# Kernel tuning notes

Measured on AMD Instinct MI355X. Metric: run time of the kernel, lower is better.

## Reference

```python
import jax, jax.numpy as jnp
import numpy as np
from jax import lax

B, H, W = 1024, 28, 28
STEPS, KMAX = 32, 2
OUT_F, NUM_CLASSES = 32, 10
P = H * W  # 784 flattened filtration values
TSEQ1 = jnp.linspace(0.01, 0.29, STEPS, dtype=jnp.float32)
TSEQ2 = jnp.linspace(0.05, 0.3, STEPS, dtype=jnp.float32)
DN = ('NHWC', 'HWIO', 'NHWC')


def setup_inputs() -> dict:
    key = jax.random.key(0)
    ks = jax.random.split(key, 16)
    return {
        'x': jax.random.normal(ks[0], (B, H, W, 1), jnp.float32),
        'x_dtm005': jax.random.uniform(ks[1], (B, H, W, 1), jnp.float32, 0.0, 0.3),
        'x_dtm02': jax.random.uniform(ks[2], (B, H, W, 1), jnp.float32, 0.0, 0.3),
        'conv_w1': jax.random.normal(ks[3], (3, 3, 1, 32), jnp.float32) * 0.1,
        'conv_b1': jnp.zeros((32,), jnp.float32),
        'conv_w2': jax.random.normal(ks[4], (3, 3, 32, 1), jnp.float32) * 0.1,
        'conv_b2': jnp.zeros((1,), jnp.float32),
        'g1_w': jax.random.normal(ks[5], (KMAX * STEPS, OUT_F), jnp.float32) * 0.1,
        'g1_b': jnp.zeros((OUT_F,), jnp.float32),
        'g2_w': jax.random.normal(ks[6], (KMAX * STEPS, OUT_F), jnp.float32) * 0.1,
        'g2_b': jnp.zeros((OUT_F,), jnp.float32),
        'fc1_w': jax.random.normal(ks[7], (P + 2 * OUT_F, 64), jnp.float32) * 0.05,
        'fc1_b': jnp.zeros((64,), jnp.float32),
        'fc2_w': jax.random.normal(ks[8], (64, NUM_CLASSES), jnp.float32) * 0.1,
        'fc2_b': jnp.zeros((NUM_CLASSES,), jnp.float32),
    }


def _landscape(v, tseq):
    """Persistence landscape over a grid of t-values.

    v: [B, P] filtration (DTM) values; each value is a birth time, paired
    with a per-sample death at the max filtration value (sublevel sweep).
    Landscape lambda_k(t) = k-th largest tent max(0, min(t-b, d-t)).
    Returns [B, KMAX*STEPS].
    """
    death = jnp.max(v, axis=1)                                     # [B]
    # tent: [B, T, P]
    tent = jnp.maximum(0.0, jnp.minimum(tseq[None, :, None] - v[:, None, :],
                                        death[:, None, None] - tseq[None, :, None]))
    top = lax.top_k(tent, KMAX)[0]                                 # [B, T, K]
    return jnp.transpose(top, (0, 2, 1)).reshape(v.shape[0], KMAX * tseq.shape[0])


def reference(x, x_dtm005, x_dtm02, conv_w1, conv_b1, conv_w2, conv_b2,
              g1_w, g1_b, g2_w, g2_b, fc1_w, fc1_b, fc2_w, fc2_b):
    b = x.shape[0]
    # TDA branch 1 (sublevel=True -> no negation)
    x1 = _landscape(x_dtm005.reshape(b, -1), TSEQ1)
    x1 = jax.nn.relu(x1 @ g1_w + g1_b)
    # TDA branch 2
    x2 = _landscape(x_dtm02.reshape(b, -1), TSEQ2)
    x2 = jax.nn.relu(x2 @ g2_w + g2_b)
    # CNN branch: Conv(32) -> ReLU -> Conv(1), then extra ReLU per call()
    h = lax.conv_general_dilated(x, conv_w1, (1, 1), 'SAME', dimension_numbers=DN) + conv_b1
    h = jax.nn.relu(h)
    h = lax.conv_general_dilated(h, conv_w2, (1, 1), 'SAME', dimension_numbers=DN) + conv_b2
    h = jax.nn.relu(h)
    hf = h.reshape(b, -1)                                          # [B, 784]
    z = jnp.concatenate([hf, x1, x2], axis=-1)                     # [B, 848]
    z = jax.nn.relu(z @ fc1_w + fc1_b)
    return z @ fc2_w + fc2_b                                       # [B, 10]
```

## Files before the change

### kernel.cpp

```cpp
#include <hip/hip_runtime.h>

#define BATCH 1024
#define PP 784

__device__ __forceinline__ float dpp_wave_shr1(float v) {
  return __int_as_float(__builtin_amdgcn_update_dpp(
      0, __float_as_int(v), 0x138, 0xF, 0xF, true));
}
__device__ __forceinline__ float dpp_wave_shl1(float v) {
  return __int_as_float(__builtin_amdgcn_update_dpp(
      0, __float_as_int(v), 0x130, 0xF, 0xF, true));
}

__global__ __launch_bounds__(512, 6) void fused_kernel(
    const float* __restrict__ xin,
    const float* __restrict__ dtm1, const float* __restrict__ dtm2,
    const float* __restrict__ w1g, const float* __restrict__ b1g,
    const float* __restrict__ w2g, const float* __restrict__ b2g,
    const float* __restrict__ g1w, const float* __restrict__ g1b,
    const float* __restrict__ g2w, const float* __restrict__ g2b,
    const float* __restrict__ fc1w, const float* __restrict__ fc1b,
    const float* __restrict__ fc2w, const float* __restrict__ fc2b,
    float* __restrict__ out)
{
  const int b = blockIdx.x;
  const int tid = threadIdx.x;
  const int w = tid >> 6;
  const int lane = tid & 63;
  const int x = lane & 31;

  __shared__ float inL[28][36];
  __shared__ __align__(16) float wTL[2][32][12];
  __shared__ float b1L[32];
  __shared__ __align__(16) float pL[8][28][28];
  __shared__ __align__(16) float zL[864];
  __shared__ float red[2][8][3];

  for (int i = tid; i < 224; i += 512) {
    int y = i >> 3, k = i & 7;
    inL[y][k == 0 ? 0 : 28 + k] = 0.f;
  }
  for (int i = tid; i < 784; i += 512)
    inL[i / 28][i % 28 + 1] = xin[b * PP + i];
  for (int i = tid; i < 288; i += 512) {
    int c = i & 31, t = i >> 5;
    wTL[0][c][t] = w1g[i];
    wTL[1][c][t] = w2g[i];
  }
  if (tid < 32) b1L[tid] = b1g[tid];
  __syncthreads();

  {
    const int sub = lane >> 5;
    float4 waA[2], waB[2], wbA[2], wbB[2];
    float wa8[2], wb8[2], bb[2];
#pragma unroll
    for (int cp = 0; cp < 2; ++cp) {
      const int c = (w << 2) + (cp << 1) + sub;
      const float* p1 = &wTL[0][c][0];
      const float* p2 = &wTL[1][c][0];
      waA[cp] = *(const float4*)p1; waB[cp] = *(const float4*)(p1 + 4); wa8[cp] = p1[8];
      wbA[cp] = *(const float4*)p2; wbB[cp] = *(const float4*)(p2 + 4); wb8[cp] = p2[8];
      bb[cp] = b1L[c];
    }

    float A0 = 0.f, A1 = 0.f, A2 = 0.f;
    float B0 = inL[0][x], B1 = inL[0][x + 1], B2 = inL[0][x + 2];
    float aM = 0.f, aC = 0.f, aP = 0.f;

#pragma unroll 2
    for (int y = 0; y < 28; ++y) {
      float C0, C1, C2;
      if (y < 27) {
        C0 = inL[y + 1][x]; C1 = inL[y + 1][x + 1]; C2 = inL[y + 1][x + 2];
      } else { C0 = 0.f; C1 = 0.f; C2 = 0.f; }

#pragma unroll
      for (int cp = 0; cp < 2; ++cp) {
        float h = bb[cp];
        h = fmaf(A0, waA[cp].x, h); h = fmaf(A1, waA[cp].y, h); h = fmaf(A2, waA[cp].z, h);
        h = fmaf(B0, waA[cp].w, h); h = fmaf(B1, waB[cp].x, h); h = fmaf(B2, waB[cp].y, h);
        h = fmaf(C0, waB[cp].z, h); h = fmaf(C1, waB[cp].w, h); h = fmaf(C2, wa8[cp], h);
        h = (x < 28) ? fmaxf(h, 0.f) : 0.f;
        float hl = dpp_wave_shr1(h);
        float hr = dpp_wave_shl1(h);
        aP = fmaf(hl, wbA[cp].x, aP); aP = fmaf(h, wbA[cp].y, aP); aP = fmaf(hr, wbA[cp].z, aP);
        aC = fmaf(hl, wbA[cp].w, aC); aC = fmaf(h, wbB[cp].x, aC); aC = fmaf(hr, wbB[cp].y, aC);
        aM = fmaf(hl, wbB[cp].z, aM); aM = fmaf(h, wbB[cp].w, aM); aM = fmaf(hr, wb8[cp], aM);
      }
      float s = aM + __shfl_xor(aM, 32);
      if (y > 0 && (lane >> 5) == 0 && x < 28) pL[w][y - 1][x] = s;
      aM = aC; aC = aP; aP = 0.f;
      A0 = B0; A1 = B1; A2 = B2;
      B0 = C0; B1 = C1; B2 = C2;
    }
    float s = aM + __shfl_xor(aM, 32);
    if ((lane >> 5) == 0 && x < 28) pL[w][27][x] = s;
  }
  __syncthreads();

  {
    const float b2v = b2g[0];
    const float* pw = (const float*)pL;
    for (int u = tid; u < 784; u += 512) {
      float v = pw[u] + pw[784 + u] + pw[1568 + u] + pw[2352 + u]
              + pw[3136 + u] + pw[3920 + u] + pw[4704 + u] + pw[5488 + u] + b2v;
      zL[u] = fmaxf(v, 0.f);
    }
  }
#pragma unroll
  for (int br = 0; br < 2; ++br) {
    float m1 = 1e30f, m2 = 1e30f, mx = -1e30f;
    if (tid < 196) {
      const float* dp = br ? dtm2 : dtm1;
      float4 x4 = *(const float4*)&dp[b * PP + tid * 4];
      float xs[4] = {x4.x, x4.y, x4.z, x4.w};
#pragma unroll
      for (int k = 0; k < 4; ++k) {
        float v = xs[k];
        mx = fmaxf(mx, v);
        float nm1 = fminf(m1, v);
        m2 = fminf(m2, fmaxf(m1, v));
        m1 = nm1;
      }
    }
#pragma unroll
    for (int off = 32; off >= 1; off >>= 1) {
      float o1 = __shfl_xor(m1, off);
      float o2 = __shfl_xor(m2, off);
      float ox = __shfl_xor(mx, off);
      mx = fmaxf(mx, ox);
      float nm1 = fminf(m1, o1);
      m2 = fminf(fminf(m2, o2), fmaxf(m1, o1));
      m1 = nm1;
    }
    if ((tid & 63) == 0) {
      red[br][w][0] = m1; red[br][w][1] = m2; red[br][w][2] = mx;
    }
  }
  __syncthreads();

  if (tid < 64) {
    const int br = tid >> 5, j = tid & 31;
    float m1 = 1e30f, m2 = 1e30f, mx = -1e30f;
#pragma unroll
    for (int wv = 0; wv < 8; ++wv) {
      float o1 = red[br][wv][0], o2 = red[br][wv][1], ox = red[br][wv][2];
      mx = fmaxf(mx, ox);
      float nm1 = fminf(m1, o1);
      m2 = fminf(fminf(m2, o2), fmaxf(m1, o1));
      m1 = nm1;
    }
    const float* gw = br ? g2w : g1w;
    const float* gb = br ? g2b : g1b;
    const float t0 = br ? 0.05f : 0.01f;
    const float dt = br ? (0.25f / 31.0f) : (0.28f / 31.0f);
    float a = gb[j];
#pragma unroll 4
    for (int i = 0; i < 64; ++i) {
      const int k = i >> 5, ti = i & 31;
      float tv = t0 + dt * (float)ti;
      float vk = k ? m2 : m1;
      float lam = fmaxf(0.0f, fminf(tv - vk, mx - tv));
      a = fmaf(lam, gw[i * 32 + j], a);
    }
    zL[784 + br * 32 + j] = fmaxf(a, 0.0f);
  }
  __syncthreads();

  float* pfcF = &pL[0][0][0];
  {
    const int part = tid >> 4, jq = tid & 15;
    const int extra = part < 20 ? part : 20;
    const int q0 = part * 6 + extra;
    const int nq = part < 20 ? 7 : 6;
    float ax = 0.f, ay = 0.f, az = 0.f, aw = 0.f;
    const int i0 = q0 * 4, i1 = i0 + nq * 4;
    for (int i = i0; i < i1; ++i) {
      float zv = zL[i];
      float4 w4 = *(const float4*)&fc1w[i * 64 + jq * 4];
      ax = fmaf(zv, w4.x, ax); ay = fmaf(zv, w4.y, ay);
      az = fmaf(zv, w4.z, az); aw = fmaf(zv, w4.w, aw);
    }
    *(float4*)&pfcF[part * 64 + jq * 4] = make_float4(ax, ay, az, aw);
  }
  __syncthreads();
  {
    float* z1L = pfcF + 2048;
    if (tid < 64) {
      float v = fc1b[tid];
#pragma unroll
      for (int p = 0; p < 32; ++p) v += pfcF[p * 64 + tid];
      z1L[tid] = fmaxf(v, 0.f);
    }
    if (tid < 10) {
      float a = fc2b[tid];
#pragma unroll 8
      for (int jj = 0; jj < 64; ++jj)
        a = fmaf(z1L[jj], fc2w[jj * 10 + tid], a);
      out[b * 10 + tid] = a;
    }
  }
}

extern "C" void kernel_launch(void* const* d_in, const int* in_sizes, int n_in,
                              void* d_out, int out_size, void* d_ws, size_t ws_size,
                              hipStream_t stream) {
  const float* x       = (const float*)d_in[0];
  const float* dtm005  = (const float*)d_in[1];
  const float* dtm02   = (const float*)d_in[2];
  const float* conv_w1 = (const float*)d_in[3];
  const float* conv_b1 = (const float*)d_in[4];
  const float* conv_w2 = (const float*)d_in[5];
  const float* conv_b2 = (const float*)d_in[6];
  const float* g1_w    = (const float*)d_in[7];
  const float* g1_b    = (const float*)d_in[8];
  const float* g2_w    = (const float*)d_in[9];
  const float* g2_b    = (const float*)d_in[10];
  const float* fc1_w   = (const float*)d_in[11];
  const float* fc1_b   = (const float*)d_in[12];
  const float* fc2_w   = (const float*)d_in[13];
  const float* fc2_b   = (const float*)d_in[14];
  float* out = (float*)d_out;

  fused_kernel<<<BATCH, 512, 0, stream>>>(
      x, dtm005, dtm02, conv_w1, conv_b1, conv_w2, conv_b2,
      g1_w, g1_b, g2_w, g2_b, fc1_w, fc1_b, fc2_w, fc2_b, out);
}
```

Before: 124.9 us.

## Restructure conv channel loop sequentially and use DPP for horizontal input neighbors

The two channel-pair iterations now run one after another with an un-unrolled outer loop, so only one channel's weights are live at a time. Partial conv2 results are stored on the first pass and accumulated in shared memory on the second. The input tile shrinks to 32 columns with zero padding, and the left and right neighbor columns come from DPP lane shifts instead of extra LDS loads. The 9-tap sum is split into three independent chains to shorten the dependency chain, the row loop is fully unrolled, and the occupancy hint in launch_bounds is dropped. The trade-off is a serialized channel loop plus read-modify-write traffic on shared memory, in exchange for lower register pressure and fewer LDS reads.

```diff
diff --git a/kernel.cpp b/kernel.cpp
--- a/kernel.cpp
+++ b/kernel.cpp
@@ -12,7 +12,7 @@
       0, __float_as_int(v), 0x130, 0xF, 0xF, true));
 }
 
-__global__ __launch_bounds__(512, 6) void fused_kernel(
+__global__ __launch_bounds__(512) void fused_kernel(
     const float* __restrict__ xin,
     const float* __restrict__ dtm1, const float* __restrict__ dtm2,
     const float* __restrict__ w1g, const float* __restrict__ b1g,
@@ -28,20 +28,19 @@
   const int w = tid >> 6;
   const int lane = tid & 63;
   const int x = lane & 31;
-
-  __shared__ float inL[28][36];
+  const int sub = lane >> 5;
+
+  __shared__ float inL[28][32];
   __shared__ __align__(16) float wTL[2][32][12];
   __shared__ float b1L[32];
   __shared__ __align__(16) float pL[8][28][28];
   __shared__ __align__(16) float zL[864];
   __shared__ float red[2][8][3];
 
-  for (int i = tid; i < 224; i += 512) {
-    int y = i >> 3, k = i & 7;
-    inL[y][k == 0 ? 0 : 28 + k] = 0.f;
-  }
-  for (int i = tid; i < 784; i += 512)
-    inL[i / 28][i % 28 + 1] = xin[b * PP + i];
+  for (int i = tid; i < 896; i += 512) {
+    int y = i >> 5, xx = i & 31;
+    inL[y][xx] = (xx < 28) ? xin[b * PP + y * 28 + xx] : 0.f;
+  }
   for (int i = tid; i < 288; i += 512) {
     int c = i & 31, t = i >> 5;
     wTL[0][c][t] = w1g[i];
@@ -50,52 +49,66 @@
   if (tid < 32) b1L[tid] = b1g[tid];
   __syncthreads();
 
-  {
-    const int sub = lane >> 5;
-    float4 waA[2], waB[2], wbA[2], wbB[2];
-    float wa8[2], wb8[2], bb[2];
-#pragma unroll
-    for (int cp = 0; cp < 2; ++cp) {
-      const int c = (w << 2) + (cp << 1) + sub;
-      const float* p1 = &wTL[0][c][0];
-      const float* p2 = &wTL[1][c][0];
-      waA[cp] = *(const float4*)p1; waB[cp] = *(const float4*)(p1 + 4); wa8[cp] = p1[8];
-      wbA[cp] = *(const float4*)p2; wbB[cp] = *(const float4*)(p2 + 4); wb8[cp] = p2[8];
-      bb[cp] = b1L[c];
-    }
+#pragma unroll 1
+  for (int cp = 0; cp < 2; ++cp) {
+    const int c = (cp << 4) + (w << 1) + sub;
+    const float* p1 = &wTL[0][c][0];
+    const float* p2 = &wTL[1][c][0];
+    float4 waA = *(const float4*)p1;
+    float4 waB = *(const float4*)(p1 + 4);
+    float  wa8 = p1[8];
+    float4 wbA = *(const float4*)p2;
+    float4 wbB = *(const float4*)(p2 + 4);
+    float  wb8 = p2[8];
+    const float bb = b1L[c];
 
     float A0 = 0.f, A1 = 0.f, A2 = 0.f;
-    float B0 = inL[0][x], B1 = inL[0][x + 1], B2 = inL[0][x + 2];
+    float B1 = inL[0][x];
+    float B0 = dpp_wave_shr1(B1), B2 = dpp_wave_shl1(B1);
     float aM = 0.f, aC = 0.f, aP = 0.f;
 
-#pragma unroll 2
+#pragma unroll
     for (int y = 0; y < 28; ++y) {
       float C0, C1, C2;
       if (y < 27) {
-        C0 = inL[y + 1][x]; C1 = inL[y + 1][x + 1]; C2 = inL[y + 1][x + 2];
+        C1 = inL[y + 1][x];
+        C0 = dpp_wave_shr1(C1);
+        C2 = dpp_wave_shl1(C1);
       } else { C0 = 0.f; C1 = 0.f; C2 = 0.f; }
 
-#pragma unroll
-      for (int cp = 0; cp < 2; ++cp) {
-        float h = bb[cp];
-        h = fmaf(A0, waA[cp].x, h); h = fmaf(A1, waA[cp].y, h); h = fmaf(A2, waA[cp].z, h);
-        h = fmaf(B0, waA[cp].w, h); h = fmaf(B1, waB[cp].x, h); h = fmaf(B2, waB[cp].y, h);
-        h = fmaf(C0, waB[cp].z, h); h = fmaf(C1, waB[cp].w, h); h = fmaf(C2, wa8[cp], h);
-        h = (x < 28) ? fmaxf(h, 0.f) : 0.f;
-        float hl = dpp_wave_shr1(h);
-        float hr = dpp_wave_shl1(h);
-        aP = fmaf(hl, wbA[cp].x, aP); aP = fmaf(h, wbA[cp].y, aP); aP = fmaf(hr, wbA[cp].z, aP);
-        aC = fmaf(hl, wbA[cp].w, aC); aC = fmaf(h, wbB[cp].x, aC); aC = fmaf(hr, wbB[cp].y, aC);
-        aM = fmaf(hl, wbB[cp].z, aM); aM = fmaf(h, wbB[cp].w, aM); aM = fmaf(hr, wb8[cp], aM);
+      float q0 = fmaf(A0, waA.x, bb);
+      q0 = fmaf(A1, waA.y, q0);
+      q0 = fmaf(A2, waA.z, q0);
+      float q1 = B0 * waA.w;
+      q1 = fmaf(B1, waB.x, q1);
+      q1 = fmaf(B2, waB.y, q1);
+      float q2 = C0 * waB.z;
+      q2 = fmaf(C1, waB.w, q2);
+      q2 = fmaf(C2, wa8, q2);
+      float h = (q0 + q1) + q2;
+      h = (x < 28) ? fmaxf(h, 0.f) : 0.f;
+      float hl = dpp_wave_shr1(h);
+      float hr = dpp_wave_shl1(h);
+      aP = fmaf(hl, wbA.x, aP); aP = fmaf(h, wbA.y, aP); aP = fmaf(hr, wbA.z, aP);
+      aC = fmaf(hl, wbA.w, aC); aC = fmaf(h, wbB.x, aC); aC = fmaf(hr, wbB.y, aC);
+      aM = fmaf(hl, wbB.z, aM); aM = fmaf(h, wbB.w, aM); aM = fmaf(hr, wb8, aM);
+
+      if (y > 0) {
+        float s = aM + __shfl_xor(aM, 32);
+        if (sub == 0 && x < 28) {
+          if (cp == 0) pL[w][y - 1][x] = s;
+          else         pL[w][y - 1][x] += s;
+        }
       }
-      float s = aM + __shfl_xor(aM, 32);
-      if (y > 0 && (lane >> 5) == 0 && x < 28) pL[w][y - 1][x] = s;
       aM = aC; aC = aP; aP = 0.f;
       A0 = B0; A1 = B1; A2 = B2;
       B0 = C0; B1 = C1; B2 = C2;
     }
     float s = aM + __shfl_xor(aM, 32);
-    if ((lane >> 5) == 0 && x < 28) pL[w][27][x] = s;
+    if (sub == 0 && x < 28) {
+      if (cp == 0) pL[w][27][x] = s;
+      else         pL[w][27][x] += s;
+    }
   }
   __syncthreads();
 
```

New measurement: 129.0 us. +3.2%, slower.
